# Kernel optimization log

Hardware: AMD Instinct MI355X
Metric: run time of the kernel (lower is better)

The kernel has to match this reference:

```python
import jax, jax.numpy as jnp
import numpy as np

M = 50000
N = 50000
H = 32
C = 128
K = 15          # sum(shell_sizes) = 1 + 14
GROUPS = 8
CPG = C // GROUPS  # 16
RADIUS = 1.2
SIGMA = 0.9
INF = 1.0e6


def _make_kernel_points():
    # fixed='center': first point at origin, rest uniformly in the ball of radius RADIUS
    rng = np.random.RandomState(42)
    pts = rng.randn(K, 3).astype(np.float32)
    pts /= np.linalg.norm(pts, axis=1, keepdims=True) + 1e-9
    r = rng.rand(K, 1).astype(np.float32) ** (1.0 / 3.0)
    pts = pts * r * RADIUS
    pts[0] = 0.0
    return jnp.asarray(pts)


def setup_inputs() -> dict:
    key = jax.random.key(0)
    ks = jax.random.split(key, 8)
    q_pts = jax.random.normal(ks[0], (M, 3), jnp.float32) * 5.0
    s_pts = q_pts + 0.0  # M == N case (same point set)
    s_feats = jax.random.normal(ks[1], (N, C), jnp.float32)
    neighb_inds = jax.random.randint(ks[2], (M, H), 0, N)
    da_scale = jax.random.uniform(ks[3], (M,), jnp.float32, 0.5, 1.5)
    # learned params
    weights = jax.random.normal(ks[4], (K, C), jnp.float32) * (1.0 / np.sqrt(C))
    w1 = jax.random.normal(ks[5], (C, C), jnp.float32) * (1.0 / np.sqrt(C))
    b1 = jnp.zeros((C,), jnp.float32)
    w2 = jax.random.normal(ks[6], (C, K * CPG), jnp.float32) * (1.0 / np.sqrt(C))
    kernel_points = _make_kernel_points()
    return {
        "q_pts": q_pts, "s_pts": s_pts, "s_feats": s_feats,
        "neighb_inds": neighb_inds, "da_scale": da_scale,
        "weights": weights, "w1": w1, "b1": b1, "w2": w2,
        "kernel_points": kernel_points,
    }


def reference(q_pts, s_pts, s_feats, neighb_inds, da_scale,
              weights, w1, b1, w2, kernel_points):
    # --- neighbor feature gather (padded shadow row of zeros) ---
    padded = jnp.concatenate([s_feats, jnp.zeros((1, C), s_feats.dtype)], axis=0)
    neighbor_feats = padded[neighb_inds]               # [M, H, C]

    # --- modulations from pooled feats (M == N -> pooled = s_feats) ---
    pooled = s_feats
    h = jax.nn.leaky_relu(pooled @ w1 + b1, 0.1)
    modulations = jax.nn.sigmoid(h @ w2)               # [M, K*CPG]
    modulations = modulations.reshape(-1, K, CPG, 1)
    conv_w = weights.reshape(1, K, CPG, GROUPS) * modulations
    conv_w = conv_w.reshape(-1, K, C)                  # [M, K, C]

    # --- density-adaptive kernel-point influences (no-grad in original) ---
    s_pad = jnp.concatenate([s_pts, jnp.full((1, 3), INF, s_pts.dtype)], axis=0)
    neighbors = s_pad[neighb_inds] - q_pts[:, None, :]            # [M, H, 3]
    scaled_kp = kernel_points[None] * da_scale[:, None, None]     # [M, K, 3]
    diff = neighbors[:, :, None, :] - scaled_kp[:, None, :, :]    # [M, H, K, 3]
    sq_d = jnp.sum(diff * diff, axis=-1)                          # [M, H, K]
    nn_sq = jnp.min(sq_d, axis=2)                                 # [M, H]
    nn_idx = jnp.argmin(sq_d, axis=2)                             # [M, H]
    infl = jnp.clip(1.0 - jnp.sqrt(nn_sq) / SIGMA, 0.0)           # linear mode
    infl = jax.lax.stop_gradient(infl)

    # --- gather per-neighbor kernel weights, modulate, aggregate ---
    nw = jnp.take_along_axis(conv_w, nn_idx[:, :, None], axis=1)  # [M, H, C]
    nw = nw * infl[:, :, None]
    return jnp.sum(neighbor_feats * nw, axis=1)                   # [M, C]
```

## Files before the change

kernel.cpp:

```cpp
#include <hip/hip_runtime.h>
#include <cstddef>
#include <cstdint>

namespace {
constexpr int H_N    = 32;
constexpr int C_F    = 128;
constexpr int K_P    = 15;
constexpr int MODC   = 240;
constexpr int ROWS_B = 64;
constexpr int LDS_SZ = ROWS_B * MODC * 2;
constexpr int QB     = 96;
}

typedef __attribute__((ext_vector_type(8))) short short8v;
typedef __attribute__((ext_vector_type(4))) float f32x4;

__device__ __forceinline__ unsigned short bf16_hi(float f) {
    unsigned u = __builtin_bit_cast(unsigned, f);
    unsigned r = (u + 0x7FFFu + ((u >> 16) & 1u)) >> 16;
    return (unsigned short)r;
}
__device__ __forceinline__ float bf16_f(unsigned short h) {
    unsigned u = ((unsigned)h) << 16;
    return __builtin_bit_cast(float, u);
}

__global__ __launch_bounds__(256)
void split_w_kernel(const float* __restrict__ w1, const float* __restrict__ w2,
                    unsigned short* __restrict__ w1t, unsigned short* __restrict__ w2t,
                    int* __restrict__ counter)
{
    const int i = blockIdx.x * 256 + threadIdx.x;
    if (i == 0) *counter = 0;
    if (i < C_F * C_F) {
        const int c = i >> 7, j = i & 127;
        w1t[j * C_F + c] = bf16_hi(w1[i]);
    }
    const int i2 = i - C_F * C_F;
    if (i2 >= 0 && i2 < C_F * MODC) {
        const int c = i2 / MODC, j = i2 - c * MODC;
        w2t[j * C_F + c] = bf16_hi(w2[i2]);
    }
}

__global__ __launch_bounds__(512, 2)
void geom_kernel(const float* __restrict__ q_pts,
                 const float* __restrict__ s_pts,
                 const int* __restrict__ nbi,
                 const float* __restrict__ da_scale,
                 const float* __restrict__ kp,
                 int* __restrict__ counter,
                 int* __restrict__ qidx,
                 unsigned* __restrict__ pk,
                 float* __restrict__ gfl,
                 float* __restrict__ out,
                 int M)
{
    __shared__ int      qidx_l[QB];
    __shared__ unsigned pk_l [QB * H_N];
    __shared__ float    gfl_l[QB * H_N];
    __shared__ int cnt_l, base_l;

    const int t    = threadIdx.x;
    const int wave = t >> 6, lane = t & 63;
    const int hl   = lane & 31;
    const int half = lane >> 5;
    const int q0   = blockIdx.x * QB;

    if (t == 0) cnt_l = 0;
    __syncthreads();

    float qx[6], qy[6], qz[6], das[6];
    int   idx[6];
    bool  valid[6];
    #pragma unroll
    for (int p = 0; p < 6; ++p) {
        const int ql = q0 + p * 16 + wave * 2 + half;
        valid[p] = ql < M;
        const int qc = valid[p] ? ql : 0;
        qx[p]  = q_pts[qc * 3 + 0];
        qy[p]  = q_pts[qc * 3 + 1];
        qz[p]  = q_pts[qc * 3 + 2];
        das[p] = da_scale[qc];
        idx[p] = nbi[(size_t)qc * H_N + hl];
    }
    float sx[6], sy[6], sz[6];
    #pragma unroll
    for (int p = 0; p < 6; ++p) {
        sx[p] = s_pts[idx[p] * 3 + 0];
        sy[p] = s_pts[idx[p] * 3 + 1];
        sz[p] = s_pts[idx[p] * 3 + 2];
    }

    #pragma unroll
    for (int p = 0; p < 6; ++p) {
        const int ql = q0 + p * 16 + wave * 2 + half;
        int   nn = 0;
        float fl = 0.f;
        if (valid[p]) {
            const float dx = __fsub_rn(sx[p], qx[p]);
            const float dy = __fsub_rn(sy[p], qy[p]);
            const float dz = __fsub_rn(sz[p], qz[p]);
            const float dd = __fadd_rn(__fadd_rn(__fmul_rn(dx, dx), __fmul_rn(dy, dy)),
                                       __fmul_rn(dz, dz));
            const float reach = 0.9f + 1.2f * das[p];
            if (dd < reach * reach) {
                float best = 3.4e38f; int bi = 0;
                #pragma unroll
                for (int k = 0; k < K_P; ++k) {
                    const float ex = __fsub_rn(dx, __fmul_rn(kp[k * 3 + 0], das[p]));
                    const float ey = __fsub_rn(dy, __fmul_rn(kp[k * 3 + 1], das[p]));
                    const float ez = __fsub_rn(dz, __fmul_rn(kp[k * 3 + 2], das[p]));
                    const float d2 = __fadd_rn(__fadd_rn(__fmul_rn(ex, ex), __fmul_rn(ey, ey)),
                                               __fmul_rn(ez, ez));
                    if (d2 < best) { best = d2; bi = k; }
                }
                const float f = 1.f - sqrtf(best) / 0.9f;
                fl = fmaxf(f, 0.f);
                nn = bi;
            }
        }

        const unsigned long long mask = __ballot(fl > 0.f);
        const unsigned long long mymask = half ? (mask & 0xFFFFFFFF00000000ull)
                                               : (mask & 0x00000000FFFFFFFFull);
        if (valid[p] && mymask == 0ull) {
            *reinterpret_cast<float4*>(out + (size_t)ql * C_F + hl * 4) =
                make_float4(0.f, 0.f, 0.f, 0.f);
        } else if (valid[p]) {
            int slot = 0;
            if (hl == 0) slot = atomicAdd(&cnt_l, 1);
            slot = __shfl(slot, half * 32);
            if (hl == 0) qidx_l[slot] = ql;
            pk_l [slot * H_N + hl] = (unsigned)idx[p] | ((unsigned)nn << 20);
            gfl_l[slot * H_N + hl] = fl;
        }
    }
    __syncthreads();

    if (t == 0) base_l = atomicAdd(counter, cnt_l);
    __syncthreads();
    const int base = base_l, cnt = cnt_l;

    for (int i = t; i < cnt; i += 512) qidx[base + i] = qidx_l[i];
    for (int i = t; i < cnt * H_N; i += 512) {
        pk [(size_t)base * H_N + i] = pk_l[i];
        gfl[(size_t)base * H_N + i] = gfl_l[i];
    }
}

__global__ __launch_bounds__(512, 2)
void active_kernel(const float* __restrict__ s_feats,
                   const float* __restrict__ weights,
                   const unsigned short* __restrict__ w1t,
                   const unsigned short* __restrict__ w2t,
                   const float* __restrict__ b1,
                   const int* __restrict__ counter,
                   const int* __restrict__ qidx,
                   const unsigned* __restrict__ pk,
                   const float* __restrict__ gfl,
                   float* __restrict__ out)
{
    __shared__ __align__(16) unsigned char lds[LDS_SZ];

    const int count = *counter;
    const int r0 = blockIdx.x * ROWS_B;
    const int rows = min(count - r0, ROWS_B);
    if (rows <= 0) return;

    const int t = threadIdx.x;
    const int wave = t >> 6, lane = t & 63;
    const int wc = wave;
    const int g  = lane >> 4;
    const int ln = lane & 15;
    const int hl   = lane & 31;
    const int half = lane >> 5;

    short8v w1f[4];
    #pragma unroll
    for (int ks = 0; ks < 4; ++ks)
        w1f[ks] = *reinterpret_cast<const short8v*>(
            w1t + (size_t)(wc * 16 + ln) * C_F + ks * 32 + g * 8);
    short8v w2f[4][2];
    #pragma unroll
    for (int ks = 0; ks < 4; ++ks) {
        #pragma unroll
        for (int cs = 0; cs < 2; ++cs) {
            const int ctile = wc + 8 * cs;
            const int colc = (ctile < K_P ? ctile : 0) * 16 + ln;
            w2f[ks][cs] = *reinterpret_cast<const short8v*>(
                w2t + (size_t)colc * C_F + ks * 32 + g * 8);
        }
    }

    unsigned pkr[4];
    float    flr[4];
    int      qir[4];
    #pragma unroll
    for (int i = 0; i < 4; ++i) {
        const int ql = i * 16 + wave * 2 + half;
        const bool v = ql < rows;
        const int pos = r0 + (v ? ql : 0);
        pkr[i] = pk[(size_t)pos * H_N + hl];
        flr[i] = v ? gfl[(size_t)pos * H_N + hl] : 0.f;
        qir[i] = qidx[pos];
    }

    {
        const int row = t >> 3;
        const int k0  = (t & 7) << 4;
        const int src_m = (row < rows) ? qidx[r0 + row] : 0;
        const float4* src = reinterpret_cast<const float4*>(
            s_feats + (size_t)src_m * C_F + k0);
        #pragma unroll
        for (int s = 0; s < 2; ++s) {
            float v[8];
            if (row < rows) {
                const float4 a = src[s * 2 + 0];
                const float4 b = src[s * 2 + 1];
                v[0] = a.x; v[1] = a.y; v[2] = a.z; v[3] = a.w;
                v[4] = b.x; v[5] = b.y; v[6] = b.z; v[7] = b.w;
            } else {
                #pragma unroll
                for (int e = 0; e < 8; ++e) v[e] = 0.f;
            }
            short8v hv;
            #pragma unroll
            for (int e = 0; e < 8; ++e) hv[e] = (short)bf16_hi(v[e]);
            const unsigned addr = (unsigned)((row * 256 + (k0 + s * 8) * 2) ^ ((row & 7) << 4));
            *reinterpret_cast<short8v*>(lds + addr) = hv;
        }
    }
    __syncthreads();

    {
        const int col = wc * 16 + ln;
        f32x4 acc[4];
        {
            const float b = b1[col];
            #pragma unroll
            for (int rt = 0; rt < 4; ++rt) acc[rt] = f32x4{b, b, b, b};
        }
        #pragma unroll
        for (int ks = 0; ks < 4; ++ks) {
            short8v a[4];
            #pragma unroll
            for (int rt = 0; rt < 4; ++rt) {
                const int row = rt * 16 + ln;
                const unsigned addr = (unsigned)((row * 256 + (ks * 32 + g * 8) * 2) ^ ((row & 7) << 4));
                a[rt] = *reinterpret_cast<const short8v*>(lds + addr);
            }
            #pragma unroll
            for (int rt = 0; rt < 4; ++rt)
                acc[rt] = __builtin_amdgcn_mfma_f32_16x16x32_bf16(a[rt], w1f[ks], acc[rt], 0, 0, 0);
        }
        __syncthreads();

        #pragma unroll
        for (int rt = 0; rt < 4; ++rt) {
            #pragma unroll
            for (int r = 0; r < 4; ++r) {
                float v = acc[rt][r];
                v = v > 0.f ? v : 0.1f * v;
                const int row = rt * 16 + g * 4 + r;
                const unsigned addr = (unsigned)((row * 256 + col * 2) ^ ((row & 7) << 4));
                *reinterpret_cast<unsigned short*>(lds + addr) = bf16_hi(v);
            }
        }
    }
    __syncthreads();

    f32x4 acc2[4][2];
    #pragma unroll
    for (int rt = 0; rt < 4; ++rt)
        #pragma unroll
        for (int cs = 0; cs < 2; ++cs) acc2[rt][cs] = f32x4{0.f, 0.f, 0.f, 0.f};

    #pragma unroll
    for (int ks = 0; ks < 4; ++ks) {
        short8v a[4];
        #pragma unroll
        for (int rt = 0; rt < 4; ++rt) {
            const int row = rt * 16 + ln;
            const unsigned addr = (unsigned)((row * 256 + (ks * 32 + g * 8) * 2) ^ ((row & 7) << 4));
            a[rt] = *reinterpret_cast<const short8v*>(lds + addr);
        }
        #pragma unroll
        for (int cs = 0; cs < 2; ++cs) {
            const int ctile = wc + 8 * cs;
            if (ctile < K_P) {
                #pragma unroll
                for (int rt = 0; rt < 4; ++rt)
                    acc2[rt][cs] = __builtin_amdgcn_mfma_f32_16x16x32_bf16(a[rt], w2f[ks][cs], acc2[rt][cs], 0, 0, 0);
            }
        }
    }
    #pragma unroll
    for (int rt = 0; rt < 4; ++rt)
        #pragma unroll
        for (int cs = 0; cs < 2; ++cs)
            #pragma unroll
            for (int r = 0; r < 4; ++r)
                acc2[rt][cs][r] = 1.f / (1.f + __expf(-acc2[rt][cs][r]));

    __syncthreads();

    #pragma unroll
    for (int rt = 0; rt < 4; ++rt) {
        #pragma unroll
        for (int cs = 0; cs < 2; ++cs) {
            const int ctile = wc + 8 * cs;
            if (ctile < K_P) {
                const int col = ctile * 16 + ln;
                #pragma unroll
                for (int r = 0; r < 4; ++r) {
                    const int row = rt * 16 + g * 4 + r;
                    *reinterpret_cast<unsigned short*>(
                        lds + row * (MODC * 2) + col * 2) = bf16_hi(acc2[rt][cs][r]);
                }
            }
        }
    }
    __syncthreads();

    const int c0 = hl << 2;
    #pragma unroll
    for (int i = 0; i < 4; ++i) {
        const int ql = i * 16 + wave * 2 + half;
        const bool valid = ql < rows;

        const int   idx = (int)(pkr[i] & 0xFFFFFu);
        const int   nn  = (int)(pkr[i] >> 20);
        const float fl  = flr[i];

        const unsigned long long mask = __ballot(fl > 0.f);
        unsigned long long mymask = half ? (mask & 0xFFFFFFFF00000000ull)
                                         : (mask & 0x00000000FFFFFFFFull);
        float4 acc = {0.f, 0.f, 0.f, 0.f};
        while (mymask) {
            const int hb = __builtin_ctzll(mymask);
            mymask &= mymask - 1;
            const int   ih = __shfl(idx, hb);
            const int   nh = __shfl(nn, hb);
            const float fh = __shfl(fl, hb);
            const float4 fv = *reinterpret_cast<const float4*>(s_feats + (size_t)ih * C_F + c0);
            const float4 wv = *reinterpret_cast<const float4*>(weights + nh * C_F + c0);
            const float  mv = bf16_f(*reinterpret_cast<const unsigned short*>(
                lds + ql * (MODC * 2) + (nh * 16 + (hl >> 1)) * 2));
            const float  s  = fh * mv;
            acc.x = fmaf(fv.x * wv.x, s, acc.x);
            acc.y = fmaf(fv.y * wv.y, s, acc.y);
            acc.z = fmaf(fv.z * wv.z, s, acc.z);
            acc.w = fmaf(fv.w * wv.w, s, acc.w);
        }
        if (valid)
            *reinterpret_cast<float4*>(out + (size_t)qir[i] * C_F + c0) = acc;
    }
}

extern "C" void kernel_launch(void* const* d_in, const int* in_sizes, int n_in,
                              void* d_out, int out_size, void* d_ws, size_t ws_size,
                              hipStream_t stream)
{
    const float* q_pts  = (const float*)d_in[0];
    const float* s_pts  = (const float*)d_in[1];
    const float* s_feat = (const float*)d_in[2];
    const int*   nbi    = (const int*)d_in[3];
    const float* da     = (const float*)d_in[4];
    const float* wts    = (const float*)d_in[5];
    const float* w1     = (const float*)d_in[6];
    const float* b1     = (const float*)d_in[7];
    const float* w2     = (const float*)d_in[8];
    const float* kp     = (const float*)d_in[9];
    float* out = (float*)d_out;

    const int M = in_sizes[4];

    unsigned short* w1t = (unsigned short*)d_ws;
    unsigned short* w2t = w1t + C_F * C_F;
    size_t off = ((size_t)(C_F * C_F + C_F * MODC) * sizeof(unsigned short) + 255) & ~(size_t)255;
    int* counter = (int*)((char*)d_ws + off);           off += 256;
    int* qidx    = (int*)((char*)d_ws + off);           off += (size_t)M * 4;
    off = (off + 255) & ~(size_t)255;
    unsigned* pk = (unsigned*)((char*)d_ws + off);      off += (size_t)M * H_N * 4;
    float* gfl   = (float*)((char*)d_ws + off);

    const int nsplit = (C_F * C_F + C_F * MODC + 255) / 256;
    split_w_kernel<<<dim3(nsplit), 256, 0, stream>>>(w1, w2, w1t, w2t, counter);

    geom_kernel<<<dim3((M + QB - 1) / QB), 512, 0, stream>>>(
        q_pts, s_pts, nbi, da, kp, counter, qidx, pk, gfl, out, M);

    active_kernel<<<dim3((M + ROWS_B - 1) / ROWS_B), 512, 0, stream>>>(
        s_feat, wts, w1t, w2t, b1, counter, qidx, pk, gfl, out);
}
```

Baseline: 41.76 us.

## Fuse geometry compaction and active-row MLP/aggregation into one kernel

Merges the geometry kernel and the active-row compute kernel into a single kernel. Each 64-query block now compacts its own active queries in LDS and runs the bf16 MFMA modulation MLP and the aggregation on them directly. This removes the global counter, the qidx/pk/gfl workspace round trip, the global atomic and one launch. The cost is that blocks with few active rows still run full-size MFMA tiles, so compute can be wasted where global compaction used to pack rows densely. LDS use per block also grows.

```diff
diff --git a/kernel.cpp b/kernel.cpp
--- a/kernel.cpp
+++ b/kernel.cpp
@@ -3,13 +3,12 @@
 #include <cstdint>
 
 namespace {
-constexpr int H_N    = 32;
-constexpr int C_F    = 128;
-constexpr int K_P    = 15;
-constexpr int MODC   = 240;
-constexpr int ROWS_B = 64;
-constexpr int LDS_SZ = ROWS_B * MODC * 2;
-constexpr int QB     = 96;
+constexpr int H_N  = 32;
+constexpr int C_F  = 128;
+constexpr int K_P  = 15;
+constexpr int MODC = 240;
+constexpr int QB   = 64;
+constexpr int TILE_SZ = QB * MODC * 2;
 }
 
 typedef __attribute__((ext_vector_type(8))) short short8v;
@@ -27,11 +26,9 @@
 
 __global__ __launch_bounds__(256)
 void split_w_kernel(const float* __restrict__ w1, const float* __restrict__ w2,
-                    unsigned short* __restrict__ w1t, unsigned short* __restrict__ w2t,
-                    int* __restrict__ counter)
+                    unsigned short* __restrict__ w1t, unsigned short* __restrict__ w2t)
 {
     const int i = blockIdx.x * 256 + threadIdx.x;
-    if (i == 0) *counter = 0;
     if (i < C_F * C_F) {
         const int c = i >> 7, j = i & 127;
         w1t[j * C_F + c] = bf16_hi(w1[i]);
@@ -44,22 +41,24 @@
 }
 
 __global__ __launch_bounds__(512, 2)
-void geom_kernel(const float* __restrict__ q_pts,
-                 const float* __restrict__ s_pts,
-                 const int* __restrict__ nbi,
-                 const float* __restrict__ da_scale,
-                 const float* __restrict__ kp,
-                 int* __restrict__ counter,
-                 int* __restrict__ qidx,
-                 unsigned* __restrict__ pk,
-                 float* __restrict__ gfl,
-                 float* __restrict__ out,
-                 int M)
+void fused_kernel(const float* __restrict__ q_pts,
+                  const float* __restrict__ s_pts,
+                  const float* __restrict__ s_feats,
+                  const int* __restrict__ nbi,
+                  const float* __restrict__ da_scale,
+                  const float* __restrict__ weights,
+                  const float* __restrict__ kp,
+                  const unsigned short* __restrict__ w1t,
+                  const unsigned short* __restrict__ w2t,
+                  const float* __restrict__ b1,
+                  float* __restrict__ out,
+                  int M)
 {
     __shared__ int      qidx_l[QB];
     __shared__ unsigned pk_l [QB * H_N];
     __shared__ float    gfl_l[QB * H_N];
-    __shared__ int cnt_l, base_l;
+    __shared__ int      cnt_l;
+    __shared__ __align__(16) unsigned char tile[TILE_SZ];
 
     const int t    = threadIdx.x;
     const int wave = t >> 6, lane = t & 63;
@@ -70,152 +69,108 @@
     if (t == 0) cnt_l = 0;
     __syncthreads();
 
-    float qx[6], qy[6], qz[6], das[6];
-    int   idx[6];
-    bool  valid[6];
-    #pragma unroll
-    for (int p = 0; p < 6; ++p) {
-        const int ql = q0 + p * 16 + wave * 2 + half;
-        valid[p] = ql < M;
-        const int qc = valid[p] ? ql : 0;
-        qx[p]  = q_pts[qc * 3 + 0];
-        qy[p]  = q_pts[qc * 3 + 1];
-        qz[p]  = q_pts[qc * 3 + 2];
-        das[p] = da_scale[qc];
-        idx[p] = nbi[(size_t)qc * H_N + hl];
-    }
-    float sx[6], sy[6], sz[6];
-    #pragma unroll
-    for (int p = 0; p < 6; ++p) {
-        sx[p] = s_pts[idx[p] * 3 + 0];
-        sy[p] = s_pts[idx[p] * 3 + 1];
-        sz[p] = s_pts[idx[p] * 3 + 2];
-    }
-
-    #pragma unroll
-    for (int p = 0; p < 6; ++p) {
-        const int ql = q0 + p * 16 + wave * 2 + half;
-        int   nn = 0;
-        float fl = 0.f;
-        if (valid[p]) {
-            const float dx = __fsub_rn(sx[p], qx[p]);
-            const float dy = __fsub_rn(sy[p], qy[p]);
-            const float dz = __fsub_rn(sz[p], qz[p]);
-            const float dd = __fadd_rn(__fadd_rn(__fmul_rn(dx, dx), __fmul_rn(dy, dy)),
-                                       __fmul_rn(dz, dz));
-            const float reach = 0.9f + 1.2f * das[p];
-            if (dd < reach * reach) {
-                float best = 3.4e38f; int bi = 0;
-                #pragma unroll
-                for (int k = 0; k < K_P; ++k) {
-                    const float ex = __fsub_rn(dx, __fmul_rn(kp[k * 3 + 0], das[p]));
-                    const float ey = __fsub_rn(dy, __fmul_rn(kp[k * 3 + 1], das[p]));
-                    const float ez = __fsub_rn(dz, __fmul_rn(kp[k * 3 + 2], das[p]));
-                    const float d2 = __fadd_rn(__fadd_rn(__fmul_rn(ex, ex), __fmul_rn(ey, ey)),
-                                               __fmul_rn(ez, ez));
-                    if (d2 < best) { best = d2; bi = k; }
-                }
-                const float f = 1.f - sqrtf(best) / 0.9f;
-                fl = fmaxf(f, 0.f);
-                nn = bi;
-            }
-        }
-
-        const unsigned long long mask = __ballot(fl > 0.f);
-        const unsigned long long mymask = half ? (mask & 0xFFFFFFFF00000000ull)
-                                               : (mask & 0x00000000FFFFFFFFull);
-        if (valid[p] && mymask == 0ull) {
-            *reinterpret_cast<float4*>(out + (size_t)ql * C_F + hl * 4) =
-                make_float4(0.f, 0.f, 0.f, 0.f);
-        } else if (valid[p]) {
-            int slot = 0;
-            if (hl == 0) slot = atomicAdd(&cnt_l, 1);
-            slot = __shfl(slot, half * 32);
-            if (hl == 0) qidx_l[slot] = ql;
-            pk_l [slot * H_N + hl] = (unsigned)idx[p] | ((unsigned)nn << 20);
-            gfl_l[slot * H_N + hl] = fl;
-        }
-    }
-    __syncthreads();
-
-    if (t == 0) base_l = atomicAdd(counter, cnt_l);
-    __syncthreads();
-    const int base = base_l, cnt = cnt_l;
-
-    for (int i = t; i < cnt; i += 512) qidx[base + i] = qidx_l[i];
-    for (int i = t; i < cnt * H_N; i += 512) {
-        pk [(size_t)base * H_N + i] = pk_l[i];
-        gfl[(size_t)base * H_N + i] = gfl_l[i];
-    }
-}
-
-__global__ __launch_bounds__(512, 2)
-void active_kernel(const float* __restrict__ s_feats,
-                   const float* __restrict__ weights,
-                   const unsigned short* __restrict__ w1t,
-                   const unsigned short* __restrict__ w2t,
-                   const float* __restrict__ b1,
-                   const int* __restrict__ counter,
-                   const int* __restrict__ qidx,
-                   const unsigned* __restrict__ pk,
-                   const float* __restrict__ gfl,
-                   float* __restrict__ out)
-{
-    __shared__ __align__(16) unsigned char lds[LDS_SZ];
-
-    const int count = *counter;
-    const int r0 = blockIdx.x * ROWS_B;
-    const int rows = min(count - r0, ROWS_B);
-    if (rows <= 0) return;
-
-    const int t = threadIdx.x;
-    const int wave = t >> 6, lane = t & 63;
-    const int wc = wave;
     const int g  = lane >> 4;
     const int ln = lane & 15;
-    const int hl   = lane & 31;
-    const int half = lane >> 5;
-
     short8v w1f[4];
     #pragma unroll
     for (int ks = 0; ks < 4; ++ks)
         w1f[ks] = *reinterpret_cast<const short8v*>(
-            w1t + (size_t)(wc * 16 + ln) * C_F + ks * 32 + g * 8);
+            w1t + (size_t)(wave * 16 + ln) * C_F + ks * 32 + g * 8);
     short8v w2f[4][2];
     #pragma unroll
     for (int ks = 0; ks < 4; ++ks) {
         #pragma unroll
         for (int cs = 0; cs < 2; ++cs) {
-            const int ctile = wc + 8 * cs;
+            const int ctile = wave + 8 * cs;
             const int colc = (ctile < K_P ? ctile : 0) * 16 + ln;
             w2f[ks][cs] = *reinterpret_cast<const short8v*>(
                 w2t + (size_t)colc * C_F + ks * 32 + g * 8);
         }
     }
 
-    unsigned pkr[4];
-    float    flr[4];
-    int      qir[4];
-    #pragma unroll
-    for (int i = 0; i < 4; ++i) {
-        const int ql = i * 16 + wave * 2 + half;
-        const bool v = ql < rows;
-        const int pos = r0 + (v ? ql : 0);
-        pkr[i] = pk[(size_t)pos * H_N + hl];
-        flr[i] = v ? gfl[(size_t)pos * H_N + hl] : 0.f;
-        qir[i] = qidx[pos];
-    }
+    {
+        float qx[4], qy[4], qz[4], das[4];
+        int   idx[4];
+        bool  valid[4];
+        #pragma unroll
+        for (int p = 0; p < 4; ++p) {
+            const int ql = q0 + p * 16 + wave * 2 + half;
+            valid[p] = ql < M;
+            const int qc = valid[p] ? ql : 0;
+            qx[p]  = q_pts[qc * 3 + 0];
+            qy[p]  = q_pts[qc * 3 + 1];
+            qz[p]  = q_pts[qc * 3 + 2];
+            das[p] = da_scale[qc];
+            idx[p] = nbi[(size_t)qc * H_N + hl];
+        }
+        float sx[4], sy[4], sz[4];
+        #pragma unroll
+        for (int p = 0; p < 4; ++p) {
+            sx[p] = s_pts[idx[p] * 3 + 0];
+            sy[p] = s_pts[idx[p] * 3 + 1];
+            sz[p] = s_pts[idx[p] * 3 + 2];
+        }
+
+        #pragma unroll
+        for (int p = 0; p < 4; ++p) {
+            const int ql = q0 + p * 16 + wave * 2 + half;
+            int   nn = 0;
+            float fl = 0.f;
+            if (valid[p]) {
+                const float dx = __fsub_rn(sx[p], qx[p]);
+                const float dy = __fsub_rn(sy[p], qy[p]);
+                const float dz = __fsub_rn(sz[p], qz[p]);
+                const float dd = __fadd_rn(__fadd_rn(__fmul_rn(dx, dx), __fmul_rn(dy, dy)),
+                                           __fmul_rn(dz, dz));
+                const float reach = 0.9f + 1.2f * das[p];
+                if (dd < reach * reach) {
+                    float best = 3.4e38f; int bi = 0;
+                    #pragma unroll
+                    for (int k = 0; k < K_P; ++k) {
+                        const float ex = __fsub_rn(dx, __fmul_rn(kp[k * 3 + 0], das[p]));
+                        const float ey = __fsub_rn(dy, __fmul_rn(kp[k * 3 + 1], das[p]));
+                        const float ez = __fsub_rn(dz, __fmul_rn(kp[k * 3 + 2], das[p]));
+                        const float d2 = __fadd_rn(__fadd_rn(__fmul_rn(ex, ex), __fmul_rn(ey, ey)),
+                                                   __fmul_rn(ez, ez));
+                        if (d2 < best) { best = d2; bi = k; }
+                    }
+                    const float f = 1.f - sqrtf(best) / 0.9f;
+                    fl = fmaxf(f, 0.f);
+                    nn = bi;
+                }
+            }
+
+            const unsigned long long mask = __ballot(fl > 0.f);
+            const unsigned long long mymask = half ? (mask & 0xFFFFFFFF00000000ull)
+                                                   : (mask & 0x00000000FFFFFFFFull);
+            if (valid[p] && mymask == 0ull) {
+                *reinterpret_cast<float4*>(out + (size_t)ql * C_F + hl * 4) =
+                    make_float4(0.f, 0.f, 0.f, 0.f);
+            } else if (valid[p]) {
+                int slot = 0;
+                if (hl == 0) slot = atomicAdd(&cnt_l, 1);
+                slot = __shfl(slot, half * 32);
+                if (hl == 0) qidx_l[slot] = ql;
+                pk_l [slot * H_N + hl] = (unsigned)idx[p] | ((unsigned)nn << 20);
+                gfl_l[slot * H_N + hl] = fl;
+            }
+        }
+    }
+    __syncthreads();
+
+    const int cnt = cnt_l;
+    if (cnt == 0) return;
 
     {
         const int row = t >> 3;
         const int k0  = (t & 7) << 4;
-        const int src_m = (row < rows) ? qidx[r0 + row] : 0;
+        const int src_m = (row < cnt) ? qidx_l[row] : 0;
         const float4* src = reinterpret_cast<const float4*>(
             s_feats + (size_t)src_m * C_F + k0);
         #pragma unroll
         for (int s = 0; s < 2; ++s) {
             float v[8];
-            if (row < rows) {
+            if (row < cnt) {
                 const float4 a = src[s * 2 + 0];
                 const float4 b = src[s * 2 + 1];
                 v[0] = a.x; v[1] = a.y; v[2] = a.z; v[3] = a.w;
@@ -228,13 +183,13 @@
             #pragma unroll
             for (int e = 0; e < 8; ++e) hv[e] = (short)bf16_hi(v[e]);
             const unsigned addr = (unsigned)((row * 256 + (k0 + s * 8) * 2) ^ ((row & 7) << 4));
-            *reinterpret_cast<short8v*>(lds + addr) = hv;
+            *reinterpret_cast<short8v*>(tile + addr) = hv;
         }
     }
     __syncthreads();
 
     {
-        const int col = wc * 16 + ln;
+        const int col = wave * 16 + ln;
         f32x4 acc[4];
         {
             const float b = b1[col];
@@ -248,7 +203,7 @@
             for (int rt = 0; rt < 4; ++rt) {
                 const int row = rt * 16 + ln;
                 const unsigned addr = (unsigned)((row * 256 + (ks * 32 + g * 8) * 2) ^ ((row & 7) << 4));
-                a[rt] = *reinterpret_cast<const short8v*>(lds + addr);
+                a[rt] = *reinterpret_cast<const short8v*>(tile + addr);
             }
             #pragma unroll
             for (int rt = 0; rt < 4; ++rt)
@@ -264,7 +219,7 @@
                 v = v > 0.f ? v : 0.1f * v;
                 const int row = rt * 16 + g * 4 + r;
                 const unsigned addr = (unsigned)((row * 256 + col * 2) ^ ((row & 7) << 4));
-                *reinterpret_cast<unsigned short*>(lds + addr) = bf16_hi(v);
+                *reinterpret_cast<unsigned short*>(tile + addr) = bf16_hi(v);
             }
         }
     }
@@ -283,11 +238,11 @@
         for (int rt = 0; rt < 4; ++rt) {
             const int row = rt * 16 + ln;
             const unsigned addr = (unsigned)((row * 256 + (ks * 32 + g * 8) * 2) ^ ((row & 7) << 4));
-            a[rt] = *reinterpret_cast<const short8v*>(lds + addr);
+            a[rt] = *reinterpret_cast<const short8v*>(tile + addr);
         }
         #pragma unroll
         for (int cs = 0; cs < 2; ++cs) {
-            const int ctile = wc + 8 * cs;
+            const int ctile = wave + 8 * cs;
             if (ctile < K_P) {
                 #pragma unroll
                 for (int rt = 0; rt < 4; ++rt)
@@ -309,14 +264,14 @@
     for (int rt = 0; rt < 4; ++rt) {
         #pragma unroll
         for (int cs = 0; cs < 2; ++cs) {
-            const int ctile = wc + 8 * cs;
+            const int ctile = wave + 8 * cs;
             if (ctile < K_P) {
                 const int col = ctile * 16 + ln;
                 #pragma unroll
                 for (int r = 0; r < 4; ++r) {
                     const int row = rt * 16 + g * 4 + r;
                     *reinterpret_cast<unsigned short*>(
-                        lds + row * (MODC * 2) + col * 2) = bf16_hi(acc2[rt][cs][r]);
+                        tile + row * (MODC * 2) + col * 2) = bf16_hi(acc2[rt][cs][r]);
                 }
             }
         }
@@ -324,14 +279,18 @@
     __syncthreads();
 
     const int c0 = hl << 2;
-    #pragma unroll
     for (int i = 0; i < 4; ++i) {
-        const int ql = i * 16 + wave * 2 + half;
-        const bool valid = ql < rows;
-
-        const int   idx = (int)(pkr[i] & 0xFFFFFu);
-        const int   nn  = (int)(pkr[i] >> 20);
-        const float fl  = flr[i];
+        const int pos = i * 16 + wave * 2 + half;
+        const bool valid = pos < cnt;
+
+        int   idx = 0, nn = 0;
+        float fl  = 0.f;
+        if (valid) {
+            const unsigned r = pk_l[pos * H_N + hl];
+            idx = (int)(r & 0xFFFFFu);
+            nn  = (int)(r >> 20);
+            fl  = gfl_l[pos * H_N + hl];
+        }
 
         const unsigned long long mask = __ballot(fl > 0.f);
         unsigned long long mymask = half ? (mask & 0xFFFFFFFF00000000ull)
@@ -346,7 +305,7 @@
             const float4 fv = *reinterpret_cast<const float4*>(s_feats + (size_t)ih * C_F + c0);
             const float4 wv = *reinterpret_cast<const float4*>(weights + nh * C_F + c0);
             const float  mv = bf16_f(*reinterpret_cast<const unsigned short*>(
-                lds + ql * (MODC * 2) + (nh * 16 + (hl >> 1)) * 2));
+                tile + pos * (MODC * 2) + (nh * 16 + (hl >> 1)) * 2));
             const float  s  = fh * mv;
             acc.x = fmaf(fv.x * wv.x, s, acc.x);
             acc.y = fmaf(fv.y * wv.y, s, acc.y);
@@ -354,7 +313,7 @@
             acc.w = fmaf(fv.w * wv.w, s, acc.w);
         }
         if (valid)
-            *reinterpret_cast<float4*>(out + (size_t)qir[i] * C_F + c0) = acc;
+            *reinterpret_cast<float4*>(out + (size_t)qidx_l[pos] * C_F + c0) = acc;
     }
 }
 
@@ -378,19 +337,10 @@
 
     unsigned short* w1t = (unsigned short*)d_ws;
     unsigned short* w2t = w1t + C_F * C_F;
-    size_t off = ((size_t)(C_F * C_F + C_F * MODC) * sizeof(unsigned short) + 255) & ~(size_t)255;
-    int* counter = (int*)((char*)d_ws + off);           off += 256;
-    int* qidx    = (int*)((char*)d_ws + off);           off += (size_t)M * 4;
-    off = (off + 255) & ~(size_t)255;
-    unsigned* pk = (unsigned*)((char*)d_ws + off);      off += (size_t)M * H_N * 4;
-    float* gfl   = (float*)((char*)d_ws + off);
 
     const int nsplit = (C_F * C_F + C_F * MODC + 255) / 256;
-    split_w_kernel<<<dim3(nsplit), 256, 0, stream>>>(w1, w2, w1t, w2t, counter);
-
-    geom_kernel<<<dim3((M + QB - 1) / QB), 512, 0, stream>>>(
-        q_pts, s_pts, nbi, da, kp, counter, qidx, pk, gfl, out, M);
-
-    active_kernel<<<dim3((M + ROWS_B - 1) / ROWS_B), 512, 0, stream>>>(
-        s_feat, wts, w1t, w2t, b1, counter, qidx, pk, gfl, out);
-}
+    split_w_kernel<<<dim3(nsplit), 256, 0, stream>>>(w1, w2, w1t, w2t);
+
+    fused_kernel<<<dim3((M + QB - 1) / QB), 512, 0, stream>>>(
+        q_pts, s_pts, s_feat, nbi, da, wts, kp, w1t, w2t, b1, out, M);
+}
```

After: 44.65 us. +6.9%, slower.
